# Optimization experiments

Measured on AMD Instinct MI355X. Metric: run time of the kernel, lower is better.

## Reference

```python
import jax, jax.numpy as jnp
import numpy as np

LOSS_WEIGHT = 1.0  # init kwarg


def _cdist2(a, b):
    # Euclidean (p=2) pairwise distances via Gram trick: avoids [n,m,d] tensor.
    d2 = (jnp.sum(a * a, axis=1)[:, None]
          + jnp.sum(b * b, axis=1)[None, :]
          - 2.0 * (a @ b.T))
    return jnp.sqrt(jnp.maximum(d2, 0.0))


def _clamp_comb(f, g):
    # Composition of clamp maps x -> clip(x, lo, hi); g is applied after f.
    lf, hf = f
    lg, hg = g
    return jnp.clip(lf, lg, hg), jnp.clip(hf, lg, hg)


def _frechet(pred, target):
    c = _cdist2(pred, target)                      # [n, m]
    # First DP row: running max of c[0, :].
    row0 = jax.lax.associative_scan(jnp.maximum, c[0])

    def row_update(prev, c_row):
        # ca[i,j] = max(min(ca[i-1,j], ca[i,j-1], ca[i-1,j-1]), c[i,j])
        # For fixed i this is d[j] = clip(d[j-1], lo=c[i,j], hi=max(b[j], c[i,j]))
        # with b[j] = min(prev[j], prev[j-1]); clamp composition is associative,
        # so the whole row is a parallel associative scan (wavefront-free form).
        d0 = jnp.maximum(prev[0], c_row[0])        # ca[i,0]
        lo = c_row[1:]
        hi = jnp.maximum(jnp.minimum(prev[1:], prev[:-1]), lo)
        lo_all = jnp.concatenate([d0[None], lo])   # element 0 is the constant map d0
        hi_all = jnp.concatenate([d0[None], hi])
        lo_s, _ = jax.lax.associative_scan(_clamp_comb, (lo_all, hi_all))
        return lo_s, None

    last_row, _ = jax.lax.scan(row_update, row0, c[1:])
    return last_row[-1]


def setup_inputs() -> dict:
    key = jax.random.key(0)
    k1, k2 = jax.random.split(key)
    pred = jax.random.uniform(k1, (4096, 128), dtype=jnp.float32)
    target = jax.random.uniform(k2, (4096, 128), dtype=jnp.float32)
    return {"pred": pred, "target": target}


def reference(pred, target):
    return LOSS_WEIGHT * _frechet(pred, target)
```

## Files before the change

### kernel.cpp

```cpp
#include <hip/hip_runtime.h>

typedef unsigned short u16;
typedef unsigned int u32;
typedef __bf16 bf16x8 __attribute__((ext_vector_type(8)));
typedef float f32x4 __attribute__((ext_vector_type(4)));

#define N 4096
#define KD 128
#define NSTRIP 32
#define G 2
#define W 128
#define ROWB 256
#define CH 32
#define NCHUNK 128
#define NBLK 130
#define TOTSTEP 4159
#define RINGROWS 128
#define WINB 32768
#define HUGEV 3.0e38f
#define TS 128
#define PADK 136

__device__ __forceinline__ u16 f2bf(float v) {
  u32 u = __float_as_uint(v);
  u += 0x7fffu + ((u >> 16) & 1u);
  return (u16)(u >> 16);
}
__device__ __forceinline__ float bf2f(u16 b) { return __uint_as_float(((u32)b) << 16); }
__device__ __forceinline__ float bfround(float v) { return bf2f(f2bf(v)); }

__device__ __forceinline__ float dpp_shr1(float oldv, float src) {
  return __int_as_float(__builtin_amdgcn_update_dpp(
      __float_as_int(oldv), __float_as_int(src), 0x138, 0xF, 0xF, false));
}

__device__ __forceinline__ void gload_lds16(const void* g, void* l) {
  __builtin_amdgcn_global_load_lds((const __attribute__((address_space(1))) u32*)g,
                                   (__attribute__((address_space(3))) u32*)l, 16, 0, 0);
}

__global__ __launch_bounds__(256) void norms_kernel(const float* __restrict__ pred,
                                                    const float* __restrict__ tgt,
                                                    float* __restrict__ na, float* __restrict__ nb,
                                                    float* __restrict__ edgeG) {
  const int t = blockIdx.x * 256 + threadIdx.x;
  if (t < NSTRIP * N) edgeG[t] = -1.0f;
  int gw = blockIdx.x * 4 + (threadIdx.x >> 6);
  int lane = threadIdx.x & 63;
  const float* base = (gw < N) ? (pred + (size_t)gw * KD) : (tgt + (size_t)(gw - N) * KD);
  float2 v = ((const float2*)base)[lane];
  float x = bfround(v.x), y = bfround(v.y);
  float s = x * x + y * y;
  #pragma unroll
  for (int off = 32; off > 0; off >>= 1) s += __shfl_xor(s, off);
  if (lane == 0) { if (gw < N) na[gw] = s; else nb[gw - N] = s; }
}

__global__ __launch_bounds__(256) void gemm_kernel(const float* __restrict__ A, const float* __restrict__ B,
                                                   const float* __restrict__ na, const float* __restrict__ nb,
                                                   u16* __restrict__ C2) {
  __shared__ u16 As[TS * PADK];
  __shared__ u16 Bs[TS * PADK];
  const int bi = blockIdx.y, bj = blockIdx.x;
  const int tid = threadIdx.x;
  {
    int row = tid >> 1, half = (tid & 1) * 64;
    const float* ga = A + (size_t)(bi * TS + row) * KD + half;
    const float* gb = B + (size_t)(bj * TS + row) * KD + half;
    u16* la = As + row * PADK + half;
    u16* lb = Bs + row * PADK + half;
    #pragma unroll
    for (int v = 0; v < 16; ++v) {
      float4 fa = ((const float4*)ga)[v];
      float4 fb = ((const float4*)gb)[v];
      *(ushort4*)(la + v * 4) = make_ushort4(f2bf(fa.x), f2bf(fa.y), f2bf(fa.z), f2bf(fa.w));
      *(ushort4*)(lb + v * 4) = make_ushort4(f2bf(fb.x), f2bf(fb.y), f2bf(fb.z), f2bf(fb.w));
    }
  }
  __syncthreads();
  const int wid = tid >> 6, lane = tid & 63;
  const int wr = (wid >> 1) * 64, wc = (wid & 1) * 64;
  const int l15 = lane & 15, l4 = lane >> 4;
  f32x4 acc[4][4] = {};
  #pragma unroll
  for (int ks = 0; ks < 4; ++ks) {
    bf16x8 af[4], bq[4];
    const int ko = ks * 32 + l4 * 8;
    #pragma unroll
    for (int m = 0; m < 4; ++m) af[m] = *(const bf16x8*)(As + (wr + m * 16 + l15) * PADK + ko);
    #pragma unroll
    for (int n = 0; n < 4; ++n) bq[n] = *(const bf16x8*)(Bs + (wc + n * 16 + l15) * PADK + ko);
    #pragma unroll
    for (int m = 0; m < 4; ++m)
      #pragma unroll
      for (int n = 0; n < 4; ++n)
        acc[m][n] = __builtin_amdgcn_mfma_f32_16x16x32_bf16(af[m], bq[n], acc[m][n], 0, 0, 0);
  }
  #pragma unroll
  for (int m = 0; m < 4; ++m) {
    const int r0 = bi * TS + wr + m * 16 + l4 * 4;
    #pragma unroll
    for (int n = 0; n < 4; ++n) {
      const int col = bj * TS + wc + n * 16 + l15;
      const float nbv = nb[col];
      #pragma unroll
      for (int e = 0; e < 4; ++e) {
        const int r = r0 + e;
        float d2v = fmaxf(na[r] + nbv - 2.0f * acc[m][n][e], 0.0f);
        C2[(size_t)r * N + col] = f2bf(d2v);
      }
    }
  }
}

#define STEP2(CU, EV) { \
  const float c0 = __uint_as_float((CU) << 16); \
  const float c1 = __uint_as_float((CU) & 0xFFFF0000u); \
  const float Lc = dpp_shr1((EV), D1); \
  const float n0 = fmaxf(c0, fminf(fminf(D0, Lp), Lc)); \
  const float n1 = fmaxf(c1, fminf(fminf(D1, D0), n0)); \
  D0 = n0; D1 = n1; Lp = Lc; \
}

#define LDGRP2(EA, EB, CV, GG) { \
  EA = *(const float4*)(elds + 8 * (GG)); \
  EB = *(const float4*)(elds + 8 * (GG) + 4); \
  CV##0 = *(const u32*)(clb + cbs); \
  CV##1 = *(const u32*)(clb + cbs + 256); \
  CV##2 = *(const u32*)(clb + cbs + 512); \
  CV##3 = *(const u32*)(clb + cbs + 768); \
  CV##4 = *(const u32*)(clb + cbs + 1024); \
  CV##5 = *(const u32*)(clb + cbs + 1280); \
  CV##6 = *(const u32*)(clb + cbs + 1536); \
  CV##7 = *(const u32*)(clb + cbs + 1792); \
  cbs += 2048; if (cbs >= WINB) cbs -= WINB; \
}

#define CGRP2(EA, EB, CV) { \
  float t0, t1, t2, t3, t4, t5, t6, t7; \
  STEP2(CV##0, EA.x); t0 = D1; \
  STEP2(CV##1, EA.y); t1 = D1; \
  STEP2(CV##2, EA.z); t2 = D1; \
  STEP2(CV##3, EA.w); t3 = D1; \
  STEP2(CV##4, EB.x); t4 = D1; \
  STEP2(CV##5, EB.y); t5 = D1; \
  STEP2(CV##6, EB.z); t6 = D1; \
  STEP2(CV##7, EB.w); t7 = D1; \
  if (e63) { \
    eout[eg + 0] = t0; eout[eg + 1] = t1; eout[eg + 2] = t2; eout[eg + 3] = t3; \
    eout[eg + 4] = t4; eout[eg + 5] = t5; eout[eg + 6] = t6; eout[eg + 7] = t7; \
  } \
  eg += 8; \
}

__global__ __launch_bounds__(64) void dp_kernel(const u16* __restrict__ C2, float* __restrict__ edgeG,
                                                float* __restrict__ out) {
  __shared__ u16 win[(RINGROWS + 8) * W];
  __shared__ __align__(16) float elds[CH];
  __shared__ __align__(16) float eout[CH];
  const int bid = blockIdx.x;
  const int S = ((bid & 7) << 2) | (bid >> 3);
  const int lane = threadIdx.x;
  const u16* cbase = C2 + (size_t)S * W;
  const char* clb = (const char*)win;
  const bool s0 = (S == 0);
  const bool do_edge = (S != NSTRIP - 1);
  const bool e63 = do_edge && (lane == 63);
  const bool l32 = lane < 32;

  if (s0 && l32) elds[lane] = (lane == 0) ? -HUGEV : HUGEV;

  float D0 = HUGEV, D1 = HUGEV, Lp = HUGEV;

  auto STAGE = [&](int c) {
    const int lrow = lane >> 4, lcol = (lane & 15) * 8;
    const u16* g0 = cbase + (size_t)(c * CH + lrow) * N + lcol;
    u16* l0 = win + (c & 3) * (CH * W);
    #pragma unroll
    for (int n = 0; n < 8; ++n) gload_lds16(g0 + (size_t)(4 * n) * N, l0 + n * 512);
    if ((c & 3) == 0) {
      u16* lm = win + RINGROWS * W;
      #pragma unroll
      for (int n = 0; n < 2; ++n) gload_lds16(g0 + (size_t)(4 * n) * N, lm + n * 512);
    }
  };

  float v0p = HUGEV;
  if (S > 0 && l32)
    v0p = __hip_atomic_fetch_add(edgeG + (size_t)(S - 1) * N + lane, 0.0f,
                                 __ATOMIC_RELAXED, __HIP_MEMORY_SCOPE_AGENT);
  STAGE(0);

  for (int q = 0; q < NBLK; ++q) {
    const int s_lo = q * CH;
    const int s_hi = (s_lo + CH < TOTSTEP) ? (s_lo + CH) : TOTSTEP;

    asm volatile("s_waitcnt vmcnt(0)" ::: "memory");
    __builtin_amdgcn_sched_barrier(0);

    if (S > 0 && q <= 127) {
      int it = 0;
      while (__any(v0p < 0.0f)) {
        __builtin_amdgcn_s_sleep(1);
        if (l32)
          v0p = __hip_atomic_fetch_add(edgeG + (size_t)(S - 1) * N + s_lo + lane, 0.0f,
                                       __ATOMIC_RELAXED, __HIP_MEMORY_SCOPE_AGENT);
        if (++it > (1 << 20)) break;
      }
      if (l32) elds[lane] = v0p;
    }
    if (s0 && q == 1 && lane == 0) elds[0] = HUGEV;

    if (S > 0 && q + 1 <= 127 && l32)
      v0p = __hip_atomic_fetch_add(edgeG + (size_t)(S - 1) * N + (q + 1) * CH + lane, 0.0f,
                                   __ATOMIC_RELAXED, __HIP_MEMORY_SCOPE_AGENT);
    else
      v0p = HUGEV;
    if (q + 1 < NCHUNK) STAGE(q + 1);

    asm volatile("s_waitcnt lgkmcnt(0)" ::: "memory");
    __builtin_amdgcn_sched_barrier(0);

    u32 cbs = (((u32)(s_lo - lane)) & 127) * ROWB + lane * (G * 2);
    int eg = 0;

    if (q >= 2 && q <= 127) {
      float4 eaA, ebA, eaB, ebB;
      u32 cA0, cA1, cA2, cA3, cA4, cA5, cA6, cA7;
      u32 cB0, cB1, cB2, cB3, cB4, cB5, cB6, cB7;
      LDGRP2(eaA, ebA, cA, 0)
      LDGRP2(eaB, ebB, cB, 1)
      CGRP2(eaA, ebA, cA)
      LDGRP2(eaA, ebA, cA, 2)
      CGRP2(eaB, ebB, cB)
      LDGRP2(eaB, ebB, cB, 3)
      CGRP2(eaA, ebA, cA)
      CGRP2(eaB, ebB, cB)
    } else {
      for (int s = s_lo; s < s_hi; ++s) {
        const u32 cu = *(const u32*)(clb + cbs);
        cbs += ROWB; if (cbs >= WINB) cbs -= WINB;
        const float ev = elds[s & (CH - 1)];
        const float c0 = __uint_as_float(cu << 16);
        const float c1 = __uint_as_float(cu & 0xFFFF0000u);
        const float Lc = dpp_shr1(ev, D1);
        const float n0 = fmaxf(c0, fminf(fminf(D0, Lp), Lc));
        const float n1 = fmaxf(c1, fminf(fminf(D1, D0), n0));
        const int ii = s - lane;
        const bool act = (u32)ii < (u32)N;
        Lp = (s0 && lane == 0) ? HUGEV : Lc;
        if (act) { D0 = n0; D1 = n1; }
        if (e63 && act) eout[s - s_lo] = n1;
      }
    }

    if (do_edge) {
      asm volatile("s_waitcnt lgkmcnt(0)" ::: "memory");
      __builtin_amdgcn_sched_barrier(0);
      const int r = s_lo - 63 + lane;
      if (l32 && r >= 0 && r < N) {
        const float v = eout[lane];
        __hip_atomic_store(edgeG + (size_t)S * N + r, v, __ATOMIC_RELAXED, __HIP_MEMORY_SCOPE_AGENT);
      }
    }
  }

  if (S == NSTRIP - 1 && lane == 63) out[0] = sqrtf(fmaxf(D1, 0.0f));
}

extern "C" void kernel_launch(void* const* d_in, const int* in_sizes, int n_in,
                              void* d_out, int out_size, void* d_ws, size_t ws_size,
                              hipStream_t stream) {
  const float* pred = (const float*)d_in[0];
  const float* tgt  = (const float*)d_in[1];
  char* ws = (char*)d_ws;
  u16* C2   = (u16*)ws;
  float* na = (float*)(ws + (size_t)N * N * 2);
  float* nb = na + N;
  float* edgeG = nb + N;
  float* out = (float*)d_out;

  hipLaunchKernelGGL(norms_kernel, dim3(2048), dim3(256), 0, stream, pred, tgt, na, nb, edgeG);
  hipLaunchKernelGGL(gemm_kernel, dim3(32, 32), dim3(256), 0, stream, pred, tgt, na, nb, C2);
  hipLaunchKernelGGL(dp_kernel, dim3(NSTRIP), dim3(64), 0, stream, C2, edgeG, out);
}
```

Measured before the change: 526.8 us.

## Store cost matrix in skewed wavefront layout and stream DP directly from global

The GEMM epilogue now writes the bf16 distance tile to LDS and re-emits it in a per-strip, anti-diagonal-skewed layout, so each DP step reads one coalesced 64-lane u32 row. The DP kernel drops the LDS ring buffer and async global-to-LDS staging and instead double-buffers register loads straight from global memory. It also broadcasts the incoming edge value with readlane instead of LDS, and writes outgoing edge values with direct atomic stores. In exchange, norms_kernel must zero the padding and the workspace grows, and per-step latency now depends on global/L2 load latency being hidden by the register prefetch.

```diff
diff --git a/kernel.cpp b/kernel.cpp
--- a/kernel.cpp
+++ b/kernel.cpp
@@ -8,15 +8,11 @@
 #define N 4096
 #define KD 128
 #define NSTRIP 32
-#define G 2
 #define W 128
-#define ROWB 256
-#define CH 32
-#define NCHUNK 128
+#define SROWS 4160
+#define SSTRIDE (SROWS * 64)
 #define NBLK 130
 #define TOTSTEP 4159
-#define RINGROWS 128
-#define WINB 32768
 #define HUGEV 3.0e38f
 #define TS 128
 #define PADK 136
@@ -34,17 +30,17 @@
       __float_as_int(oldv), __float_as_int(src), 0x138, 0xF, 0xF, false));
 }
 
-__device__ __forceinline__ void gload_lds16(const void* g, void* l) {
-  __builtin_amdgcn_global_load_lds((const __attribute__((address_space(1))) u32*)g,
-                                   (__attribute__((address_space(3))) u32*)l, 16, 0, 0);
-}
-
 __global__ __launch_bounds__(256) void norms_kernel(const float* __restrict__ pred,
                                                     const float* __restrict__ tgt,
                                                     float* __restrict__ na, float* __restrict__ nb,
-                                                    float* __restrict__ edgeG) {
+                                                    float* __restrict__ edgeG, u32* __restrict__ C2T) {
   const int t = blockIdx.x * 256 + threadIdx.x;
   if (t < NSTRIP * N) edgeG[t] = -1.0f;
+  if (t < NSTRIP * 8192) {
+    const int strip = t >> 13, idx = t & 8191;
+    const int s = (idx < 4096) ? (idx >> 6) : (4095 + ((idx - 4096) >> 6));
+    C2T[(size_t)strip * SSTRIDE + s * 64 + (idx & 63)] = 0;
+  }
   int gw = blockIdx.x * 4 + (threadIdx.x >> 6);
   int lane = threadIdx.x & 63;
   const float* base = (gw < N) ? (pred + (size_t)gw * KD) : (tgt + (size_t)(gw - N) * KD);
@@ -58,7 +54,7 @@
 
 __global__ __launch_bounds__(256) void gemm_kernel(const float* __restrict__ A, const float* __restrict__ B,
                                                    const float* __restrict__ na, const float* __restrict__ nb,
-                                                   u16* __restrict__ C2) {
+                                                   u32* __restrict__ C2T) {
   __shared__ u16 As[TS * PADK];
   __shared__ u16 Bs[TS * PADK];
   const int bi = blockIdx.y, bj = blockIdx.x;
@@ -96,176 +92,147 @@
       for (int n = 0; n < 4; ++n)
         acc[m][n] = __builtin_amdgcn_mfma_f32_16x16x32_bf16(af[m], bq[n], acc[m][n], 0, 0, 0);
   }
+  __syncthreads();
   #pragma unroll
   for (int m = 0; m < 4; ++m) {
-    const int r0 = bi * TS + wr + m * 16 + l4 * 4;
+    const int rl0 = wr + m * 16 + l4 * 4;
     #pragma unroll
     for (int n = 0; n < 4; ++n) {
-      const int col = bj * TS + wc + n * 16 + l15;
-      const float nbv = nb[col];
+      const int cl = wc + n * 16 + l15;
+      const float nbv = nb[bj * TS + cl];
       #pragma unroll
       for (int e = 0; e < 4; ++e) {
-        const int r = r0 + e;
-        float d2v = fmaxf(na[r] + nbv - 2.0f * acc[m][n][e], 0.0f);
-        C2[(size_t)r * N + col] = f2bf(d2v);
+        const int rl = rl0 + e;
+        float d2v = fmaxf(na[bi * TS + rl] + nbv - 2.0f * acc[m][n][e], 0.0f);
+        As[rl * PADK + cl] = f2bf(d2v);
       }
     }
   }
-}
-
-#define STEP2(CU, EV) { \
+  __syncthreads();
+  const u32* Tp = (const u32*)As;
+  u32* outb = C2T + (size_t)bj * SSTRIDE + (size_t)(bi * TS) * 64 + lane;
+  #pragma unroll 1
+  for (int k = 0; k < 48; ++k) {
+    const int sl = wid + 4 * k;
+    if (sl < 191) {
+      const int rl = sl - lane;
+      if ((u32)rl < 128u) outb[sl * 64] = Tp[rl * 68 + lane];
+    }
+  }
+}
+
+#define STEP1(CU, IDX) { \
+  const float ev = __int_as_float(__builtin_amdgcn_readlane(__float_as_int(vUse), (IDX))); \
+  const float evv = lane0 ? ev : 0.0f; \
+  const float Lc = dpp_shr1(evv, D1); \
   const float c0 = __uint_as_float((CU) << 16); \
   const float c1 = __uint_as_float((CU) & 0xFFFF0000u); \
-  const float Lc = dpp_shr1((EV), D1); \
   const float n0 = fmaxf(c0, fminf(fminf(D0, Lp), Lc)); \
   const float n1 = fmaxf(c1, fminf(fminf(D1, D0), n0)); \
   D0 = n0; D1 = n1; Lp = Lc; \
 }
 
-#define LDGRP2(EA, EB, CV, GG) { \
-  EA = *(const float4*)(elds + 8 * (GG)); \
-  EB = *(const float4*)(elds + 8 * (GG) + 4); \
-  CV##0 = *(const u32*)(clb + cbs); \
-  CV##1 = *(const u32*)(clb + cbs + 256); \
-  CV##2 = *(const u32*)(clb + cbs + 512); \
-  CV##3 = *(const u32*)(clb + cbs + 768); \
-  CV##4 = *(const u32*)(clb + cbs + 1024); \
-  CV##5 = *(const u32*)(clb + cbs + 1280); \
-  CV##6 = *(const u32*)(clb + cbs + 1536); \
-  CV##7 = *(const u32*)(clb + cbs + 1792); \
-  cbs += 2048; if (cbs >= WINB) cbs -= WINB; \
-}
-
-#define CGRP2(EA, EB, CV) { \
+#define LDV(V) { \
+  V##0 = pld[0];   V##1 = pld[64];  V##2 = pld[128]; V##3 = pld[192]; \
+  V##4 = pld[256]; V##5 = pld[320]; V##6 = pld[384]; V##7 = pld[448]; \
+  pld += 512; \
+}
+
+#define EST(p, v) __hip_atomic_store((p), (v), __ATOMIC_RELAXED, __HIP_MEMORY_SCOPE_AGENT)
+
+#define CG(V, G0) { \
   float t0, t1, t2, t3, t4, t5, t6, t7; \
-  STEP2(CV##0, EA.x); t0 = D1; \
-  STEP2(CV##1, EA.y); t1 = D1; \
-  STEP2(CV##2, EA.z); t2 = D1; \
-  STEP2(CV##3, EA.w); t3 = D1; \
-  STEP2(CV##4, EB.x); t4 = D1; \
-  STEP2(CV##5, EB.y); t5 = D1; \
-  STEP2(CV##6, EB.z); t6 = D1; \
-  STEP2(CV##7, EB.w); t7 = D1; \
-  if (e63) { \
-    eout[eg + 0] = t0; eout[eg + 1] = t1; eout[eg + 2] = t2; eout[eg + 3] = t3; \
-    eout[eg + 4] = t4; eout[eg + 5] = t5; eout[eg + 6] = t6; eout[eg + 7] = t7; \
+  STEP1(V##0, (G0) + 0); t0 = D1; \
+  STEP1(V##1, (G0) + 1); t1 = D1; \
+  STEP1(V##2, (G0) + 2); t2 = D1; \
+  STEP1(V##3, (G0) + 3); t3 = D1; \
+  STEP1(V##4, (G0) + 4); t4 = D1; \
+  STEP1(V##5, (G0) + 5); t5 = D1; \
+  STEP1(V##6, (G0) + 6); t6 = D1; \
+  STEP1(V##7, (G0) + 7); t7 = D1; \
+  if (e63q2) { \
+    float* ea = eB + (q * 32 - 63 + (G0)); \
+    EST(ea + 0, t0); EST(ea + 1, t1); EST(ea + 2, t2); EST(ea + 3, t3); \
+    EST(ea + 4, t4); EST(ea + 5, t5); EST(ea + 6, t6); EST(ea + 7, t7); \
+  } else if (e63 && q == 1 && (G0) == 24) { \
+    EST(eB, t7); \
   } \
-  eg += 8; \
-}
-
-__global__ __launch_bounds__(64) void dp_kernel(const u16* __restrict__ C2, float* __restrict__ edgeG,
+}
+
+__global__ __launch_bounds__(64) void dp_kernel(const u32* __restrict__ C2T, float* __restrict__ edgeG,
                                                 float* __restrict__ out) {
-  __shared__ u16 win[(RINGROWS + 8) * W];
-  __shared__ __align__(16) float elds[CH];
-  __shared__ __align__(16) float eout[CH];
   const int bid = blockIdx.x;
   const int S = ((bid & 7) << 2) | (bid >> 3);
   const int lane = threadIdx.x;
-  const u16* cbase = C2 + (size_t)S * W;
-  const char* clb = (const char*)win;
-  const bool s0 = (S == 0);
+  const bool lane0 = (lane == 0);
+  const u32* cb = C2T + (size_t)S * SSTRIDE + lane;
+  float* eB = edgeG + (size_t)S * N;
+  float* eI = edgeG + (size_t)(S - 1) * N;
+  const bool sp = (S > 0);
   const bool do_edge = (S != NSTRIP - 1);
   const bool e63 = do_edge && (lane == 63);
   const bool l32 = lane < 32;
 
-  if (s0 && l32) elds[lane] = (lane == 0) ? -HUGEV : HUGEV;
-
-  float D0 = HUGEV, D1 = HUGEV, Lp = HUGEV;
-
-  auto STAGE = [&](int c) {
-    const int lrow = lane >> 4, lcol = (lane & 15) * 8;
-    const u16* g0 = cbase + (size_t)(c * CH + lrow) * N + lcol;
-    u16* l0 = win + (c & 3) * (CH * W);
-    #pragma unroll
-    for (int n = 0; n < 8; ++n) gload_lds16(g0 + (size_t)(4 * n) * N, l0 + n * 512);
-    if ((c & 3) == 0) {
-      u16* lm = win + RINGROWS * W;
-      #pragma unroll
-      for (int n = 0; n < 2; ++n) gload_lds16(g0 + (size_t)(4 * n) * N, lm + n * 512);
-    }
-  };
-
+  float D0 = HUGEV, D1 = HUGEV;
+  float Lp = (S == 0 && lane == 0) ? -HUGEV : HUGEV;
   float v0p = HUGEV;
-  if (S > 0 && l32)
-    v0p = __hip_atomic_fetch_add(edgeG + (size_t)(S - 1) * N + lane, 0.0f,
-                                 __ATOMIC_RELAXED, __HIP_MEMORY_SCOPE_AGENT);
-  STAGE(0);
-
-  for (int q = 0; q < NBLK; ++q) {
-    const int s_lo = q * CH;
-    const int s_hi = (s_lo + CH < TOTSTEP) ? (s_lo + CH) : TOTSTEP;
-
-    asm volatile("s_waitcnt vmcnt(0)" ::: "memory");
-    __builtin_amdgcn_sched_barrier(0);
-
-    if (S > 0 && q <= 127) {
+  if (sp && l32)
+    v0p = __hip_atomic_fetch_add(eI + lane, 0.0f, __ATOMIC_RELAXED, __HIP_MEMORY_SCOPE_AGENT);
+
+  const u32* pld = cb;
+  u32 A0, A1, A2, A3, A4, A5, A6, A7;
+  u32 B0, B1, B2, B3, B4, B5, B6, B7;
+  LDV(A)
+  LDV(B)
+
+  #pragma unroll 1
+  for (int q = 0; q < 129; ++q) {
+    if (sp && q <= 127) {
       int it = 0;
       while (__any(v0p < 0.0f)) {
         __builtin_amdgcn_s_sleep(1);
         if (l32)
-          v0p = __hip_atomic_fetch_add(edgeG + (size_t)(S - 1) * N + s_lo + lane, 0.0f,
+          v0p = __hip_atomic_fetch_add(eI + q * 32 + lane, 0.0f,
                                        __ATOMIC_RELAXED, __HIP_MEMORY_SCOPE_AGENT);
         if (++it > (1 << 20)) break;
       }
-      if (l32) elds[lane] = v0p;
-    }
-    if (s0 && q == 1 && lane == 0) elds[0] = HUGEV;
-
-    if (S > 0 && q + 1 <= 127 && l32)
-      v0p = __hip_atomic_fetch_add(edgeG + (size_t)(S - 1) * N + (q + 1) * CH + lane, 0.0f,
+    }
+    const float vUse = v0p;
+    if (sp && q + 1 <= 127 && l32)
+      v0p = __hip_atomic_fetch_add(eI + (q + 1) * 32 + lane, 0.0f,
                                    __ATOMIC_RELAXED, __HIP_MEMORY_SCOPE_AGENT);
-    else
-      v0p = HUGEV;
-    if (q + 1 < NCHUNK) STAGE(q + 1);
-
-    asm volatile("s_waitcnt lgkmcnt(0)" ::: "memory");
-    __builtin_amdgcn_sched_barrier(0);
-
-    u32 cbs = (((u32)(s_lo - lane)) & 127) * ROWB + lane * (G * 2);
-    int eg = 0;
-
-    if (q >= 2 && q <= 127) {
-      float4 eaA, ebA, eaB, ebB;
-      u32 cA0, cA1, cA2, cA3, cA4, cA5, cA6, cA7;
-      u32 cB0, cB1, cB2, cB3, cB4, cB5, cB6, cB7;
-      LDGRP2(eaA, ebA, cA, 0)
-      LDGRP2(eaB, ebB, cB, 1)
-      CGRP2(eaA, ebA, cA)
-      LDGRP2(eaA, ebA, cA, 2)
-      CGRP2(eaB, ebB, cB)
-      LDGRP2(eaB, ebB, cB, 3)
-      CGRP2(eaA, ebA, cA)
-      CGRP2(eaB, ebB, cB)
-    } else {
-      for (int s = s_lo; s < s_hi; ++s) {
-        const u32 cu = *(const u32*)(clb + cbs);
-        cbs += ROWB; if (cbs >= WINB) cbs -= WINB;
-        const float ev = elds[s & (CH - 1)];
-        const float c0 = __uint_as_float(cu << 16);
-        const float c1 = __uint_as_float(cu & 0xFFFF0000u);
-        const float Lc = dpp_shr1(ev, D1);
-        const float n0 = fmaxf(c0, fminf(fminf(D0, Lp), Lc));
-        const float n1 = fmaxf(c1, fminf(fminf(D1, D0), n0));
-        const int ii = s - lane;
-        const bool act = (u32)ii < (u32)N;
-        Lp = (s0 && lane == 0) ? HUGEV : Lc;
-        if (act) { D0 = n0; D1 = n1; }
-        if (e63 && act) eout[s - s_lo] = n1;
+    const bool e63q2 = e63 && (q >= 2);
+
+    CG(A, 0)  LDV(A)
+    CG(B, 8)  LDV(B)
+    CG(A, 16) LDV(A)
+    CG(B, 24) LDV(B)
+  }
+
+  {
+    const int q = 129;
+    const float vUse = v0p;
+    const bool e63q2 = e63;
+    CG(A, 0)  LDV(A)
+    CG(B, 8)  LDV(B)
+    CG(A, 16)
+    {
+      float t0, t1, t2, t3, t4, t5, t6;
+      STEP1(B0, 24); t0 = D1;
+      STEP1(B1, 25); t1 = D1;
+      STEP1(B2, 26); t2 = D1;
+      STEP1(B3, 27); t3 = D1;
+      STEP1(B4, 28); t4 = D1;
+      STEP1(B5, 29); t5 = D1;
+      STEP1(B6, 30); t6 = D1;
+      if (e63q2) {
+        float* ea = eB + (q * 32 - 63 + 24);
+        EST(ea + 0, t0); EST(ea + 1, t1); EST(ea + 2, t2); EST(ea + 3, t3);
+        EST(ea + 4, t4); EST(ea + 5, t5); EST(ea + 6, t6);
       }
-    }
-
-    if (do_edge) {
-      asm volatile("s_waitcnt lgkmcnt(0)" ::: "memory");
-      __builtin_amdgcn_sched_barrier(0);
-      const int r = s_lo - 63 + lane;
-      if (l32 && r >= 0 && r < N) {
-        const float v = eout[lane];
-        __hip_atomic_store(edgeG + (size_t)S * N + r, v, __ATOMIC_RELAXED, __HIP_MEMORY_SCOPE_AGENT);
-      }
-    }
-  }
-
-  if (S == NSTRIP - 1 && lane == 63) out[0] = sqrtf(fmaxf(D1, 0.0f));
+      if (S == NSTRIP - 1 && lane == 63) out[0] = sqrtf(fmaxf(t6, 0.0f));
+    }
+  }
 }
 
 extern "C" void kernel_launch(void* const* d_in, const int* in_sizes, int n_in,
@@ -274,13 +241,13 @@
   const float* pred = (const float*)d_in[0];
   const float* tgt  = (const float*)d_in[1];
   char* ws = (char*)d_ws;
-  u16* C2   = (u16*)ws;
-  float* na = (float*)(ws + (size_t)N * N * 2);
+  u32* C2T  = (u32*)ws;
+  float* na = (float*)(ws + (size_t)NSTRIP * SSTRIDE * 4);
   float* nb = na + N;
   float* edgeG = nb + N;
   float* out = (float*)d_out;
 
-  hipLaunchKernelGGL(norms_kernel, dim3(2048), dim3(256), 0, stream, pred, tgt, na, nb, edgeG);
-  hipLaunchKernelGGL(gemm_kernel, dim3(32, 32), dim3(256), 0, stream, pred, tgt, na, nb, C2);
-  hipLaunchKernelGGL(dp_kernel, dim3(NSTRIP), dim3(64), 0, stream, C2, edgeG, out);
-}
+  hipLaunchKernelGGL(norms_kernel, dim3(2048), dim3(256), 0, stream, pred, tgt, na, nb, edgeG, C2T);
+  hipLaunchKernelGGL(gemm_kernel, dim3(32, 32), dim3(256), 0, stream, pred, tgt, na, nb, C2T);
+  hipLaunchKernelGGL(dp_kernel, dim3(NSTRIP), dim3(64), 0, stream, C2T, edgeG, out);
+}
```

Result: slower. 545.1 us (+3.5%).

## Process 2x2 DP cell block per lane per step to halve wavefront steps

Applied to the files above, without the earlier changes.

Restructures the strip DP so each lane advances two rows and two columns per step instead of one row, halving the number of sequential wavefront steps per chunk (16 steps per 32 rows). It enlarges the LDS ring to 256 rows, removes the mirrored tail rows, and reworks the edge output buffer into a 64-entry ring with new indexing. The cost is a longer per-step dependency chain and more complex boundary and edge handling, along with more pipeline fill and drain chunks.

```diff
diff --git a/kernel.cpp b/kernel.cpp
--- a/kernel.cpp
+++ b/kernel.cpp
@@ -8,15 +8,11 @@
 #define N 4096
 #define KD 128
 #define NSTRIP 32
-#define G 2
 #define W 128
 #define ROWB 256
 #define CH 32
-#define NCHUNK 128
-#define NBLK 130
-#define TOTSTEP 4159
-#define RINGROWS 128
-#define WINB 32768
+#define STB 16
+#define NBLK 132
 #define HUGEV 3.0e38f
 #define TS 128
 #define PADK 136
@@ -113,51 +109,48 @@
   }
 }
 
-#define STEP2(CU, EV) { \
-  const float c0 = __uint_as_float((CU) << 16); \
-  const float c1 = __uint_as_float((CU) & 0xFFFF0000u); \
-  const float Lc = dpp_shr1((EV), D1); \
-  const float n0 = fmaxf(c0, fminf(fminf(D0, Lp), Lc)); \
-  const float n1 = fmaxf(c1, fminf(fminf(D1, D0), n0)); \
-  D0 = n0; D1 = n1; Lp = Lc; \
-}
-
-#define LDGRP2(EA, EB, CV, GG) { \
-  EA = *(const float4*)(elds + 8 * (GG)); \
-  EB = *(const float4*)(elds + 8 * (GG) + 4); \
-  CV##0 = *(const u32*)(clb + cbs); \
-  CV##1 = *(const u32*)(clb + cbs + 256); \
-  CV##2 = *(const u32*)(clb + cbs + 512); \
-  CV##3 = *(const u32*)(clb + cbs + 768); \
-  CV##4 = *(const u32*)(clb + cbs + 1024); \
-  CV##5 = *(const u32*)(clb + cbs + 1280); \
-  CV##6 = *(const u32*)(clb + cbs + 1536); \
-  CV##7 = *(const u32*)(clb + cbs + 1792); \
-  cbs += 2048; if (cbs >= WINB) cbs -= WINB; \
-}
-
-#define CGRP2(EA, EB, CV) { \
-  float t0, t1, t2, t3, t4, t5, t6, t7; \
-  STEP2(CV##0, EA.x); t0 = D1; \
-  STEP2(CV##1, EA.y); t1 = D1; \
-  STEP2(CV##2, EA.z); t2 = D1; \
-  STEP2(CV##3, EA.w); t3 = D1; \
-  STEP2(CV##4, EB.x); t4 = D1; \
-  STEP2(CV##5, EB.y); t5 = D1; \
-  STEP2(CV##6, EB.z); t6 = D1; \
-  STEP2(CV##7, EB.w); t7 = D1; \
-  if (e63) { \
-    eout[eg + 0] = t0; eout[eg + 1] = t1; eout[eg + 2] = t2; eout[eg + 3] = t3; \
-    eout[eg + 4] = t4; eout[eg + 5] = t5; eout[eg + 6] = t6; eout[eg + 7] = t7; \
-  } \
-  eg += 8; \
+#define STEPR2(CU0, CU1, EAv, EBv) { \
+  const float La = dpp_shr1((EAv), E0); \
+  const float Lb = dpp_shr1((EBv), D1); \
+  const float c00 = __uint_as_float((CU0) << 16); \
+  const float c01 = __uint_as_float((CU0) & 0xFFFF0000u); \
+  const float c10 = __uint_as_float((CU1) << 16); \
+  const float c11 = __uint_as_float((CU1) & 0xFFFF0000u); \
+  const float o00 = fmaxf(c00, fminf(fminf(D0, Lbp), La)); \
+  const float o01 = fmaxf(c01, fminf(fminf(D1, D0), o00)); \
+  const float o10 = fmaxf(c10, fminf(fminf(o00, La), Lb)); \
+  const float o11 = fmaxf(c11, fminf(fminf(o01, o00), o10)); \
+  D0 = o10; D1 = o11; E0 = o01; Lbp = Lb; \
+}
+
+#define EOUTW { \
+  if (e63) { eout[eix] = E0; eout[eix + 1] = D1; } \
+  eix = (eix + 2) & 63; \
+}
+
+#define LDGR(EA4, EB4, CV, GG) { \
+  EA4 = *(const float4*)(elds + 8 * (GG)); \
+  EB4 = *(const float4*)(elds + 8 * (GG) + 4); \
+  { const u32 a0 = cbs, a1 = (cbs + 512) & 0xFFFFu, a2 = (cbs + 1024) & 0xFFFFu, a3 = (cbs + 1536) & 0xFFFFu; \
+    CV##u0 = *(const u32*)(clb + a0); CV##v0 = *(const u32*)(clb + a0 + 256); \
+    CV##u1 = *(const u32*)(clb + a1); CV##v1 = *(const u32*)(clb + a1 + 256); \
+    CV##u2 = *(const u32*)(clb + a2); CV##v2 = *(const u32*)(clb + a2 + 256); \
+    CV##u3 = *(const u32*)(clb + a3); CV##v3 = *(const u32*)(clb + a3 + 256); } \
+  cbs = (cbs + 2048) & 0xFFFFu; \
+}
+
+#define CGR(EA4, EB4, CV) { \
+  STEPR2(CV##u0, CV##v0, EA4.x, EA4.y) EOUTW \
+  STEPR2(CV##u1, CV##v1, EA4.z, EA4.w) EOUTW \
+  STEPR2(CV##u2, CV##v2, EB4.x, EB4.y) EOUTW \
+  STEPR2(CV##u3, CV##v3, EB4.z, EB4.w) EOUTW \
 }
 
 __global__ __launch_bounds__(64) void dp_kernel(const u16* __restrict__ C2, float* __restrict__ edgeG,
                                                 float* __restrict__ out) {
-  __shared__ u16 win[(RINGROWS + 8) * W];
-  __shared__ __align__(16) float elds[CH];
-  __shared__ __align__(16) float eout[CH];
+  __shared__ u16 win[256 * W];
+  __shared__ __align__(16) float elds[32];
+  __shared__ __align__(16) float eout[64];
   const int bid = blockIdx.x;
   const int S = ((bid & 7) << 2) | (bid >> 3);
   const int lane = threadIdx.x;
@@ -167,34 +160,28 @@
   const bool do_edge = (S != NSTRIP - 1);
   const bool e63 = do_edge && (lane == 63);
   const bool l32 = lane < 32;
-
-  if (s0 && l32) elds[lane] = (lane == 0) ? -HUGEV : HUGEV;
-
-  float D0 = HUGEV, D1 = HUGEV, Lp = HUGEV;
+  float* eB = edgeG + (size_t)S * N;
+  float* eI = edgeG + (size_t)(S - 1) * N;
+
+  if (s0 && l32) elds[lane] = HUGEV;
+
+  float D0 = HUGEV, D1 = HUGEV, E0 = HUGEV;
+  float Lbp = (s0 && lane == 0) ? -HUGEV : HUGEV;
 
   auto STAGE = [&](int c) {
     const int lrow = lane >> 4, lcol = (lane & 15) * 8;
     const u16* g0 = cbase + (size_t)(c * CH + lrow) * N + lcol;
-    u16* l0 = win + (c & 3) * (CH * W);
+    u16* l0 = win + ((c & 7) * CH) * W;
     #pragma unroll
     for (int n = 0; n < 8; ++n) gload_lds16(g0 + (size_t)(4 * n) * N, l0 + n * 512);
-    if ((c & 3) == 0) {
-      u16* lm = win + RINGROWS * W;
-      #pragma unroll
-      for (int n = 0; n < 2; ++n) gload_lds16(g0 + (size_t)(4 * n) * N, lm + n * 512);
-    }
   };
 
   float v0p = HUGEV;
   if (S > 0 && l32)
-    v0p = __hip_atomic_fetch_add(edgeG + (size_t)(S - 1) * N + lane, 0.0f,
-                                 __ATOMIC_RELAXED, __HIP_MEMORY_SCOPE_AGENT);
+    v0p = __hip_atomic_fetch_add(eI + lane, 0.0f, __ATOMIC_RELAXED, __HIP_MEMORY_SCOPE_AGENT);
   STAGE(0);
 
   for (int q = 0; q < NBLK; ++q) {
-    const int s_lo = q * CH;
-    const int s_hi = (s_lo + CH < TOTSTEP) ? (s_lo + CH) : TOTSTEP;
-
     asm volatile("s_waitcnt vmcnt(0)" ::: "memory");
     __builtin_amdgcn_sched_barrier(0);
 
@@ -203,64 +190,70 @@
       while (__any(v0p < 0.0f)) {
         __builtin_amdgcn_s_sleep(1);
         if (l32)
-          v0p = __hip_atomic_fetch_add(edgeG + (size_t)(S - 1) * N + s_lo + lane, 0.0f,
+          v0p = __hip_atomic_fetch_add(eI + q * 32 + lane, 0.0f,
                                        __ATOMIC_RELAXED, __HIP_MEMORY_SCOPE_AGENT);
         if (++it > (1 << 20)) break;
       }
       if (l32) elds[lane] = v0p;
     }
-    if (s0 && q == 1 && lane == 0) elds[0] = HUGEV;
 
     if (S > 0 && q + 1 <= 127 && l32)
-      v0p = __hip_atomic_fetch_add(edgeG + (size_t)(S - 1) * N + (q + 1) * CH + lane, 0.0f,
+      v0p = __hip_atomic_fetch_add(eI + (q + 1) * 32 + lane, 0.0f,
                                    __ATOMIC_RELAXED, __HIP_MEMORY_SCOPE_AGENT);
     else
       v0p = HUGEV;
-    if (q + 1 < NCHUNK) STAGE(q + 1);
+    if (q + 1 < 128) STAGE(q + 1);
 
     asm volatile("s_waitcnt lgkmcnt(0)" ::: "memory");
     __builtin_amdgcn_sched_barrier(0);
 
-    u32 cbs = (((u32)(s_lo - lane)) & 127) * ROWB + lane * (G * 2);
-    int eg = 0;
-
-    if (q >= 2 && q <= 127) {
-      float4 eaA, ebA, eaB, ebB;
-      u32 cA0, cA1, cA2, cA3, cA4, cA5, cA6, cA7;
-      u32 cB0, cB1, cB2, cB3, cB4, cB5, cB6, cB7;
-      LDGRP2(eaA, ebA, cA, 0)
-      LDGRP2(eaB, ebB, cB, 1)
-      CGRP2(eaA, ebA, cA)
-      LDGRP2(eaA, ebA, cA, 2)
-      CGRP2(eaB, ebB, cB)
-      LDGRP2(eaB, ebB, cB, 3)
-      CGRP2(eaA, ebA, cA)
-      CGRP2(eaB, ebB, cB)
+    u32 cbs = (((u32)(32 * q - 2 * lane)) & 255u) * ROWB + lane * 4;
+    int eix = (32 * q - 126) & 63;
+
+    if (q >= 4 && q <= 127) {
+      float4 Aea, Aeb, Bea, Beb;
+      u32 Au0, Av0, Au1, Av1, Au2, Av2, Au3, Av3;
+      u32 Bu0, Bv0, Bu1, Bv1, Bu2, Bv2, Bu3, Bv3;
+      LDGR(Aea, Aeb, A, 0)
+      LDGR(Bea, Beb, B, 1)
+      CGR(Aea, Aeb, A)
+      LDGR(Aea, Aeb, A, 2)
+      CGR(Bea, Beb, B)
+      LDGR(Bea, Beb, B, 3)
+      CGR(Aea, Aeb, A)
+      CGR(Bea, Beb, B)
     } else {
-      for (int s = s_lo; s < s_hi; ++s) {
-        const u32 cu = *(const u32*)(clb + cbs);
-        cbs += ROWB; if (cbs >= WINB) cbs -= WINB;
-        const float ev = elds[s & (CH - 1)];
-        const float c0 = __uint_as_float(cu << 16);
-        const float c1 = __uint_as_float(cu & 0xFFFF0000u);
-        const float Lc = dpp_shr1(ev, D1);
-        const float n0 = fmaxf(c0, fminf(fminf(D0, Lp), Lc));
-        const float n1 = fmaxf(c1, fminf(fminf(D1, D0), n0));
-        const int ii = s - lane;
-        const bool act = (u32)ii < (u32)N;
-        Lp = (s0 && lane == 0) ? HUGEV : Lc;
-        if (act) { D0 = n0; D1 = n1; }
-        if (e63 && act) eout[s - s_lo] = n1;
+      for (int k = 0; k < STB; ++k) {
+        const int s = STB * q + k;
+        const int i0 = 2 * (s - lane);
+        const bool act = (u32)i0 <= 4094u;
+        const u32 cu0 = *(const u32*)(clb + cbs);
+        const u32 cu1 = *(const u32*)(clb + cbs + 256);
+        cbs = (cbs + 512) & 0xFFFFu;
+        const float ea = elds[(2 * k) & 31];
+        const float eb = elds[(2 * k + 1) & 31];
+        const float La = dpp_shr1(ea, E0);
+        const float Lb = dpp_shr1(eb, D1);
+        const float c00 = __uint_as_float(cu0 << 16);
+        const float c01 = __uint_as_float(cu0 & 0xFFFF0000u);
+        const float c10 = __uint_as_float(cu1 << 16);
+        const float c11 = __uint_as_float(cu1 & 0xFFFF0000u);
+        const float o00 = fmaxf(c00, fminf(fminf(D0, Lbp), La));
+        const float o01 = fmaxf(c01, fminf(fminf(D1, D0), o00));
+        const float o10 = fmaxf(c10, fminf(fminf(o00, La), Lb));
+        const float o11 = fmaxf(c11, fminf(fminf(o01, o00), o10));
+        if (act) { D0 = o10; D1 = o11; E0 = o01; Lbp = Lb; }
+        if (e63 && act) { eout[i0 & 63] = o01; eout[(i0 + 1) & 63] = o11; }
       }
     }
 
     if (do_edge) {
       asm volatile("s_waitcnt lgkmcnt(0)" ::: "memory");
       __builtin_amdgcn_sched_barrier(0);
-      const int r = s_lo - 63 + lane;
+      const int r = 32 * q - 126 + lane;
       if (l32 && r >= 0 && r < N) {
-        const float v = eout[lane];
-        __hip_atomic_store(edgeG + (size_t)S * N + r, v, __ATOMIC_RELAXED, __HIP_MEMORY_SCOPE_AGENT);
+        const float v = eout[r & 63];
+        __hip_atomic_store(eB + r, v, __ATOMIC_RELAXED, __HIP_MEMORY_SCOPE_AGENT);
       }
     }
   }
```

Result: slower. 597.4 us (+13.4%).
